# Optimization experiments

Measured on AMD Instinct MI355X. Metric: run time of the kernel, lower is better.

Reference implementation:

```python
import jax, jax.numpy as jnp
import numpy as np

T = 32          # timesteps
GAIN = 1.0      # input_gain
TAU = 2.0       # LIF membrane time constant
VTH = 1.0       # v_threshold
VRESET = 0.0    # v_reset (hard reset)
ALPHA = 2.0     # ATan surrogate alpha


@jax.custom_vjp
def heaviside_atan(x):
    # forward: Heaviside spike; backward: ATan surrogate gradient
    return (x >= 0).astype(x.dtype)

def _hs_fwd(x):
    return heaviside_atan(x), x

def _hs_bwd(x, g):
    # d/dx ATan surrogate: (alpha/2) / (1 + (pi/2 * alpha * x)^2)
    return (g * (ALPHA / 2.0) / (1.0 + (jnp.pi / 2.0 * ALPHA * x) ** 2),)

heaviside_atan.defvjp(_hs_fwd, _hs_bwd)


def lif_multistep(cur_seq):
    """Multi-step LIF over cur_seq [T, B, H]; hard reset, detach_reset=True."""
    def step(v, x):
        # charge: v = v + (x - (v - v_reset)) / tau
        v = v + (x - (v - VRESET)) / TAU
        spike = heaviside_atan(v - VTH)
        sd = jax.lax.stop_gradient(spike)  # detach_reset
        v = (1.0 - sd) * v + sd * VRESET   # hard reset
        return v, spike

    v0 = jnp.full(cur_seq.shape[1:], VRESET, dtype=cur_seq.dtype)
    _, spikes = jax.lax.scan(step, v0, cur_seq)
    return spikes


def setup_inputs() -> dict:
    key = jax.random.key(0)
    ks = jax.random.split(key, 4)

    def xavier(k, o, i):
        lim = np.sqrt(6.0 / (i + o)).astype(np.float32)
        return jax.random.uniform(k, (o, i), minval=-lim, maxval=lim, dtype=jnp.float32)

    x_flat = jax.random.uniform(ks[0], (512, 784), dtype=jnp.float32)
    W0 = xavier(ks[1], 1024, 784)
    b0 = jnp.zeros((1024,), jnp.float32)
    W1 = xavier(ks[2], 1024, 1024)
    b1 = jnp.zeros((1024,), jnp.float32)
    W2 = xavier(ks[3], 10, 1024)
    b2 = jnp.zeros((10,), jnp.float32)
    return {"x_flat": x_flat, "W0": W0, "b0": b0, "W1": W1, "b1": b1, "W2": W2, "b2": b2}


def reference(x_flat, W0, b0, W1, b1, W2, b2):
    # repeat_static_input: [B, 784] -> [T, B, 784]
    h = jnp.broadcast_to(x_flat * GAIN, (T,) + x_flat.shape)
    count = None
    for W, b in ((W0, b0), (W1, b1), (W2, b2)):
        cur = jnp.einsum('tbi,oi->tbo', h, W) + b  # fc over all timesteps
        spk = lif_multistep(cur)                   # [T, B, out]
        count = spk.sum(axis=0)                    # spike counts [B, out]
        h = spk
    # predict() returns argmax(count); return the final count (logits) here
    return count
```

## Files before the change

### kernel.cpp

```cpp
#include <hip/hip_runtime.h>
#include <hip/hip_bf16.h>
#include <stdint.h>


typedef __bf16 bf16x8 __attribute__((ext_vector_type(8)));
typedef float  f32x4  __attribute__((ext_vector_type(4)));

__device__ __forceinline__ void gload16(const void* g, void* l) {
  __builtin_amdgcn_global_load_lds((const __attribute__((address_space(1))) void*)g,
                                   (__attribute__((address_space(3))) void*)l,
                                   16, 0, 0);
}

__device__ __forceinline__ void bsplit3(float v, __hip_bfloat16& h,
                                        __hip_bfloat16& m, __hip_bfloat16& l) {
  h = __float2bfloat16(v);
  float r1 = v - __bfloat162float(h);
  m = __float2bfloat16(r1);
  float r2 = r1 - __bfloat162float(m);
  l = __float2bfloat16(r2);
}

__global__ __launch_bounds__(256) void prep_k(const float* __restrict__ x,
                                              const float* __restrict__ W0,
                                              const float* __restrict__ W1,
                                              __hip_bfloat16* __restrict__ Ax,
                                              __hip_bfloat16* __restrict__ Bw,
                                              float* __restrict__ W1T) {
  const int bid = blockIdx.x, tid = threadIdx.x;
  if (bid < 1600) {
    int i = bid * 256 + tid;
    int m = i / 800, k = i - m * 800;
    float v = (k < 784) ? x[(size_t)m * 784 + k] : 0.f;
    __hip_bfloat16 h, mm, l;
    bsplit3(v, h, mm, l);
    size_t base = (size_t)m * 4800;
    Ax[base + k] = h;         Ax[base + 800 + k] = h;
    Ax[base + 1600 + k] = mm; Ax[base + 2400 + k] = mm;
    Ax[base + 3200 + k] = h;  Ax[base + 4000 + k] = l;
  } else if (bid < 4800) {
    int i = (bid - 1600) * 256 + tid;
    int n = i / 800, k = i - n * 800;
    float v = (k < 784) ? W0[(size_t)n * 784 + k] : 0.f;
    __hip_bfloat16 h, mm, l;
    bsplit3(v, h, mm, l);
    size_t base = (size_t)n * 4800;
    Bw[base + k] = h;         Bw[base + 800 + k] = mm;
    Bw[base + 1600 + k] = h;  Bw[base + 2400 + k] = mm;
    Bw[base + 3200 + k] = l;  Bw[base + 4000 + k] = h;
  } else {
    __shared__ float t[32][33];
    int tt = bid - 4800;
    int c0 = (tt & 31) * 32, r0 = (tt >> 5) * 32;
    int lx = tid & 31, ly = tid >> 5;
#pragma unroll
    for (int i = 0; i < 32; i += 8)
      t[ly + i][lx] = W1[(size_t)(r0 + ly + i) * 1024 + (c0 + lx)];
    __syncthreads();
#pragma unroll
    for (int i = 0; i < 32; i += 8)
      W1T[(size_t)(c0 + ly + i) * 1024 + (r0 + lx)] = t[lx][ly + i];
  }
}

__global__ __launch_bounds__(256, 2) void gemm0_k(const __hip_bfloat16* __restrict__ A,
                                                  const __hip_bfloat16* __restrict__ B,
                                                  float* __restrict__ Cpart) {
  __shared__ __align__(16) __hip_bfloat16 As[128 * 32];
  __shared__ __align__(16) __hip_bfloat16 Bs[128 * 32];
  const int tid = threadIdx.x;
  const int wave = tid >> 6, lane = tid & 63, quad = lane >> 4, l16 = lane & 15;
  const int wm = (wave >> 1) * 64, wn = (wave & 1) * 64;
  const int mbase = blockIdx.x * 128, nbase = blockIdx.y * 128;
  const int kbase = blockIdx.z * 480;
  const int srow = lane >> 2;
  const int gq = (lane & 3) ^ ((lane >> 3) & 3);
  const int swz = (l16 >> 1) & 3;
  f32x4 acc[4][4] = {};
  for (int kk = kbase; kk < kbase + 480; kk += 32) {
#pragma unroll
    for (int r = 0; r < 2; ++r) {
      int grp = wave * 2 + r;
      gload16(A + (size_t)(mbase + grp * 16 + srow) * 4800 + kk + gq * 8,
              (char*)As + grp * 1024);
      gload16(B + (size_t)(nbase + grp * 16 + srow) * 4800 + kk + gq * 8,
              (char*)Bs + grp * 1024);
    }
    __syncthreads();
    const __bf16* Ab = (const __bf16*)As;
    const __bf16* Bb = (const __bf16*)Bs;
    bf16x8 af[4], bfr[4];
#pragma unroll
    for (int i = 0; i < 4; ++i)
      af[i] = *(const bf16x8*)(Ab + (wm + i * 16 + l16) * 32 + ((quad ^ swz) * 8));
#pragma unroll
    for (int j = 0; j < 4; ++j)
      bfr[j] = *(const bf16x8*)(Bb + (wn + j * 16 + l16) * 32 + ((quad ^ swz) * 8));
#pragma unroll
    for (int i = 0; i < 4; ++i)
#pragma unroll
      for (int j = 0; j < 4; ++j)
        acc[i][j] = __builtin_amdgcn_mfma_f32_16x16x32_bf16(af[i], bfr[j], acc[i][j], 0, 0, 0);
    __syncthreads();
  }
  float* Cz = Cpart + (size_t)blockIdx.z * 512 * 1024;
#pragma unroll
  for (int i = 0; i < 4; ++i)
#pragma unroll
    for (int j = 0; j < 4; ++j)
#pragma unroll
      for (int r = 0; r < 4; ++r) {
        int m = mbase + wm + i * 16 + quad * 4 + r;
        int n = nbase + wn + j * 16 + l16;
        Cz[(size_t)m * 1024 + n] = acc[i][j][r];
      }
}

__global__ __launch_bounds__(1024) void compact0_k(const float* __restrict__ Cpart,
                                                   const float* __restrict__ b0,
                                                   unsigned short* __restrict__ lidx16,
                                                   int* __restrict__ segs) {
  __shared__ int whist[16][33];
  __shared__ int clstot[33];
  __shared__ int clsofs[34];
  __shared__ int wofs[16][33];
  int b = blockIdx.x, o = threadIdx.x;
  int wave = o >> 6, lane = o & 63;
  float cur = 0.f;
#pragma unroll
  for (int z = 0; z < 10; ++z)
    cur += Cpart[(size_t)z * 512 * 1024 + (size_t)b * 1024 + o];
  cur += b0[o];
  float v = 0.f;
  unsigned word = 0u;
#pragma unroll
  for (int t = 0; t < 32; ++t) {
    v = v + (cur - v) * 0.5f;
    if (v >= 1.0f) { word |= 1u << t; v = 0.f; }
  }
  int n = word ? (__builtin_ctz(word) + 1) : 0;
  unsigned long long mymask = 0ull;
#pragma unroll 1
  for (int c = 1; c <= 32; ++c) {
    unsigned long long m = __ballot(n == c);
    if (lane == 0) whist[wave][c] = __popcll(m);
    if (n == c) mymask = m;
  }
  __syncthreads();
  if (o < 32) {
    int c = o + 1, s = 0;
#pragma unroll
    for (int w = 0; w < 16; ++w) s += whist[w][c];
    clstot[c] = s;
  }
  __syncthreads();
  if (o == 0) {
    int run = 0;
#pragma unroll
    for (int c = 1; c <= 32; ++c) { clsofs[c] = run; run += clstot[c]; }
    clsofs[33] = run;
  }
  __syncthreads();
  if (o < 32) {
    int c = o + 1, s = clsofs[c];
#pragma unroll
    for (int w = 0; w < 16; ++w) { wofs[w][c] = s; s += whist[w][c]; }
  }
  __syncthreads();
  if (n) {
    int pos = wofs[wave][n] + __popcll(mymask & ((1ull << lane) - 1ull));
    lidx16[(size_t)b * 1024 + pos] = (unsigned short)o;
  }
  if (o < 33) segs[b * 33 + o] = clsofs[o + 1];
}

__global__ __launch_bounds__(256) void layer1_k(const unsigned short* __restrict__ lidx16,
                                                const int* __restrict__ segs,
                                                const float* __restrict__ W1T,
                                                const float* __restrict__ b1,
                                                unsigned* __restrict__ l2idx,
                                                unsigned* __restrict__ l2wrd,
                                                int* __restrict__ n2t) {
  __shared__ unsigned short sidx[1024];
  __shared__ int sseg[33];
  __shared__ int wtot[4], wbase[4];
  const int tile = blockIdx.x, b = blockIdx.y;
  const int tid = threadIdx.x;
  const int o = tile * 256 + tid;
  if (tid < 33) sseg[tid] = segs[b * 33 + tid];
  __syncthreads();
  const int total = __builtin_amdgcn_readfirstlane(sseg[32]);
  for (int i = tid; i < total; i += 256)
    sidx[i] = lidx16[(size_t)b * 1024 + i];
  __syncthreads();
  float S[32];
#pragma unroll
  for (int c = 0; c < 32; ++c) {
    int j0 = __builtin_amdgcn_readfirstlane((c == 0) ? 0 : sseg[c - 1]);
    int j1 = __builtin_amdgcn_readfirstlane(sseg[c]);
    float s = 0.f;
    for (int j = j0; j < j1; ++j)
      s += W1T[(size_t)sidx[j] * 1024 + o];
    S[c] = s;
  }
  const float bias = b1[o];
  float v = 0.f;
  unsigned word = 0u;
#pragma unroll
  for (int t = 0; t < 32; ++t) {
    float cur = 0.f;
#pragma unroll
    for (int c = 1; c <= 32; ++c)
      if ((t + 1) % c == 0) cur += S[c - 1];
    float xc = cur + bias;
    v = v + (xc - v) * 0.5f;
    if (v >= 1.0f) { word |= 1u << t; v = 0.f; }
  }
  bool act = (word != 0u);
  unsigned long long m = __ballot(act);
  int wave = tid >> 6, lane = tid & 63;
  if (lane == 0) wtot[wave] = __popcll(m);
  __syncthreads();
  if (tid == 0) {
    int s = 0;
#pragma unroll
    for (int i = 0; i < 4; ++i) { wbase[i] = s; s += wtot[i]; }
    n2t[b * 4 + tile] = s;
  }
  __syncthreads();
  if (act) {
    int pos = wbase[wave] + __popcll(m & ((1ull << lane) - 1ull));
    l2idx[(size_t)b * 1024 + tile * 256 + pos] = (unsigned)o;
    l2wrd[(size_t)b * 1024 + tile * 256 + pos] = word;
  }
}

__global__ __launch_bounds__(320) void layer2_k(const unsigned* __restrict__ l2idx,
                                                const unsigned* __restrict__ l2wrd,
                                                const int* __restrict__ n2t,
                                                const float* __restrict__ W2,
                                                const float* __restrict__ b2,
                                                float* __restrict__ out) {
  __shared__ float sW2[10 * 1025];
  __shared__ unsigned sidx[1024], swrd[1024];
  __shared__ float scur[320];
  int b = blockIdx.x, tid = threadIdx.x;
  int cnt[4], ofs[4], mtot = 0;
#pragma unroll
  for (int s = 0; s < 4; ++s) {
    cnt[s] = n2t[b * 4 + s];
    ofs[s] = mtot;
    mtot += cnt[s];
  }
  for (int i = tid; i < 10240; i += 320)
    sW2[(i >> 10) * 1025 + (i & 1023)] = W2[i];
#pragma unroll
  for (int s = 0; s < 4; ++s)
    for (int i = tid; i < cnt[s]; i += 320) {
      sidx[ofs[s] + i] = l2idx[(size_t)b * 1024 + s * 256 + i];
      swrd[ofs[s] + i] = l2wrd[(size_t)b * 1024 + s * 256 + i];
    }
  __syncthreads();
  int t = tid / 10, c = tid - t * 10;
  float acc = 0.f;
  for (int j = 0; j < mtot; ++j) {
    unsigned wd = swrd[j];
    float wv = sW2[c * 1025 + sidx[j]];
    acc += ((wd >> t) & 1u) ? wv : 0.f;
  }
  scur[t * 10 + c] = acc;
  __syncthreads();
  if (tid < 10) {
    float v = 0.f, cnt2 = 0.f, bias = b2[tid];
#pragma unroll
    for (int tt = 0; tt < 32; ++tt) {
      float xc = scur[tt * 10 + tid] + bias;
      v = v + (xc - v) * 0.5f;
      if (v >= 1.0f) { cnt2 += 1.f; v = 0.f; }
    }
    out[(size_t)b * 10 + tid] = cnt2;
  }
}

extern "C" void kernel_launch(void* const* d_in, const int* in_sizes, int n_in,
                              void* d_out, int out_size, void* d_ws, size_t ws_size,
                              hipStream_t stream) {
  const float* x  = (const float*)d_in[0];
  const float* W0 = (const float*)d_in[1];
  const float* b0 = (const float*)d_in[2];
  const float* W1 = (const float*)d_in[3];
  const float* b1 = (const float*)d_in[4];
  const float* W2 = (const float*)d_in[5];
  const float* b2 = (const float*)d_in[6];
  float* out = (float*)d_out;

  char* ws = (char*)d_ws;
  size_t off = 0;
  auto alloc = [&](size_t bytes) -> char* {
    char* p = ws + off;
    off += (bytes + 255) & ~(size_t)255;
    return p;
  };
  __hip_bfloat16* Ax     = (__hip_bfloat16*)alloc((size_t)512 * 4800 * 2);
  __hip_bfloat16* Bw     = (__hip_bfloat16*)alloc((size_t)1024 * 4800 * 2);
  float*          Cpart  = (float*)alloc((size_t)10 * 512 * 1024 * 4);
  float*          W1T    = (float*)alloc((size_t)1024 * 1024 * 4);
  unsigned short* lidx16 = (unsigned short*)alloc((size_t)512 * 1024 * 2);
  int*            segs   = (int*)alloc((size_t)512 * 33 * 4);
  unsigned*       l2idx  = (unsigned*)alloc((size_t)512 * 1024 * 4);
  unsigned*       l2wrd  = (unsigned*)alloc((size_t)512 * 1024 * 4);
  int*            n2t    = (int*)alloc((size_t)512 * 4 * 4);
  (void)ws_size;

  prep_k<<<5824, 256, 0, stream>>>(x, W0, W1, Ax, Bw, W1T);
  gemm0_k<<<dim3(4, 8, 10), 256, 0, stream>>>(Ax, Bw, Cpart);
  compact0_k<<<512, 1024, 0, stream>>>(Cpart, b0, lidx16, segs);
  layer1_k<<<dim3(4, 512), 256, 0, stream>>>(lidx16, segs, W1T, b1, l2idx, l2wrd, n2t);
  layer2_k<<<512, 320, 0, stream>>>(l2idx, l2wrd, n2t, W2, b2, out);
}
```

Measured before the change: 117.7 us.

## Fuse bf16 split into GEMM loads and merge tail kernels into one

The GEMM now reads fp32 x and W0 directly, performs the three-way bf16 split on the fly, and writes swizzled tiles to LDS, replacing the separate prep pass and its large bf16 workspace. The W1 transpose runs as extra blocks of the same launch. Compaction, layer 1 and layer 2 are fused into one 1024-thread-per-batch kernel that keeps its intermediates in shared memory. This cuts kernel launches and global round-trips, but the GEMM loses asynchronous global-to-LDS loads and repeats the split arithmetic per tile, and layer 1 now runs on 512 blocks instead of 2048.

```diff
diff --git a/kernel.cpp b/kernel.cpp
--- a/kernel.cpp
+++ b/kernel.cpp
@@ -5,52 +5,30 @@
 
 typedef __bf16 bf16x8 __attribute__((ext_vector_type(8)));
 typedef float  f32x4  __attribute__((ext_vector_type(4)));
-
-__device__ __forceinline__ void gload16(const void* g, void* l) {
-  __builtin_amdgcn_global_load_lds((const __attribute__((address_space(1))) void*)g,
-                                   (__attribute__((address_space(3))) void*)l,
-                                   16, 0, 0);
+typedef unsigned short u16x8 __attribute__((ext_vector_type(8)));
+
+__device__ __forceinline__ unsigned short csel(float v, int sel) {
+  __hip_bfloat16 h = __float2bfloat16(v);
+  if (sel == 0) return __builtin_bit_cast(unsigned short, h);
+  float r1 = v - __bfloat162float(h);
+  __hip_bfloat16 m = __float2bfloat16(r1);
+  if (sel == 1) return __builtin_bit_cast(unsigned short, m);
+  float r2 = r1 - __bfloat162float(m);
+  __hip_bfloat16 l = __float2bfloat16(r2);
+  return __builtin_bit_cast(unsigned short, l);
 }
 
-__device__ __forceinline__ void bsplit3(float v, __hip_bfloat16& h,
-                                        __hip_bfloat16& m, __hip_bfloat16& l) {
-  h = __float2bfloat16(v);
-  float r1 = v - __bfloat162float(h);
-  m = __float2bfloat16(r1);
-  float r2 = r1 - __bfloat162float(m);
-  l = __float2bfloat16(r2);
-}
-
-__global__ __launch_bounds__(256) void prep_k(const float* __restrict__ x,
-                                              const float* __restrict__ W0,
-                                              const float* __restrict__ W1,
-                                              __hip_bfloat16* __restrict__ Ax,
-                                              __hip_bfloat16* __restrict__ Bw,
-                                              float* __restrict__ W1T) {
+__global__ __launch_bounds__(256, 2) void gemm0t_k(const float* __restrict__ x,
+                                                   const float* __restrict__ W0,
+                                                   const float* __restrict__ W1,
+                                                   float* __restrict__ W1T,
+                                                   float* __restrict__ Cpart) {
+  __shared__ __align__(16) char smem[16512];
   const int bid = blockIdx.x, tid = threadIdx.x;
-  if (bid < 1600) {
-    int i = bid * 256 + tid;
-    int m = i / 800, k = i - m * 800;
-    float v = (k < 784) ? x[(size_t)m * 784 + k] : 0.f;
-    __hip_bfloat16 h, mm, l;
-    bsplit3(v, h, mm, l);
-    size_t base = (size_t)m * 4800;
-    Ax[base + k] = h;         Ax[base + 800 + k] = h;
-    Ax[base + 1600 + k] = mm; Ax[base + 2400 + k] = mm;
-    Ax[base + 3200 + k] = h;  Ax[base + 4000 + k] = l;
-  } else if (bid < 4800) {
-    int i = (bid - 1600) * 256 + tid;
-    int n = i / 800, k = i - n * 800;
-    float v = (k < 784) ? W0[(size_t)n * 784 + k] : 0.f;
-    __hip_bfloat16 h, mm, l;
-    bsplit3(v, h, mm, l);
-    size_t base = (size_t)n * 4800;
-    Bw[base + k] = h;         Bw[base + 800 + k] = mm;
-    Bw[base + 1600 + k] = h;  Bw[base + 2400 + k] = mm;
-    Bw[base + 3200 + k] = l;  Bw[base + 4000 + k] = h;
-  } else {
-    __shared__ float t[32][33];
-    int tt = bid - 4800;
+
+  if (bid >= 320) {
+    float (*t)[33] = (float(*)[33])smem;
+    int tt = bid - 320;
     int c0 = (tt & 31) * 32, r0 = (tt >> 5) * 32;
     int lx = tid & 31, ly = tid >> 5;
 #pragma unroll
@@ -60,35 +38,74 @@
 #pragma unroll
     for (int i = 0; i < 32; i += 8)
       W1T[(size_t)(c0 + ly + i) * 1024 + (r0 + lx)] = t[lx][ly + i];
-  }
-}
-
-__global__ __launch_bounds__(256, 2) void gemm0_k(const __hip_bfloat16* __restrict__ A,
-                                                  const __hip_bfloat16* __restrict__ B,
-                                                  float* __restrict__ Cpart) {
-  __shared__ __align__(16) __hip_bfloat16 As[128 * 32];
-  __shared__ __align__(16) __hip_bfloat16 Bs[128 * 32];
-  const int tid = threadIdx.x;
+    return;
+  }
+
+  const int bx = bid & 3, by = (bid >> 2) & 7, bz = bid >> 5;
   const int wave = tid >> 6, lane = tid & 63, quad = lane >> 4, l16 = lane & 15;
   const int wm = (wave >> 1) * 64, wn = (wave & 1) * 64;
-  const int mbase = blockIdx.x * 128, nbase = blockIdx.y * 128;
-  const int kbase = blockIdx.z * 480;
-  const int srow = lane >> 2;
-  const int gq = (lane & 3) ^ ((lane >> 3) & 3);
+  const int mbase = bx * 128, nbase = by * 128, kbase = bz * 480;
   const int swz = (l16 >> 1) & 3;
+
+  const int r = tid >> 1, h = tid & 1;
+  const int sw = (r >> 1) & 3;
+  const int swap = sw & 1;
+  char* adst = smem + r * 64 + 32 * (h ^ (sw >> 1));
+  char* bdst = smem + 8192 + r * 64 + 32 * (h ^ (sw >> 1));
+  const float* xr = x + (size_t)(mbase + r) * 784;
+  const float* wr = W0 + (size_t)(nbase + r) * 784;
+
   f32x4 acc[4][4] = {};
+
   for (int kk = kbase; kk < kbase + 480; kk += 32) {
-#pragma unroll
-    for (int r = 0; r < 2; ++r) {
-      int grp = wave * 2 + r;
-      gload16(A + (size_t)(mbase + grp * 16 + srow) * 4800 + kk + gq * 8,
-              (char*)As + grp * 1024);
-      gload16(B + (size_t)(nbase + grp * 16 + srow) * 4800 + kk + gq * 8,
-              (char*)Bs + grp * 1024);
-    }
-    __syncthreads();
-    const __bf16* Ab = (const __bf16*)As;
-    const __bf16* Bb = (const __bf16*)Bs;
+    const int s = kk / 800;
+    const int k0 = kk - s * 800 + h * 16;
+    const int selA = (s == 2 || s == 3) ? 1 : ((s == 5) ? 2 : 0);
+    const int selB = (s == 1 || s == 3) ? 1 : ((s == 4) ? 2 : 0);
+    {
+      float v[16];
+#pragma unroll
+      for (int q = 0; q < 4; ++q) {
+        int kq = k0 + q * 4;
+        if (kq < 784) {
+          f32x4 t4 = *(const f32x4*)(xr + kq);
+          v[q*4+0] = t4[0]; v[q*4+1] = t4[1]; v[q*4+2] = t4[2]; v[q*4+3] = t4[3];
+        } else {
+          v[q*4+0] = 0.f; v[q*4+1] = 0.f; v[q*4+2] = 0.f; v[q*4+3] = 0.f;
+        }
+      }
+      u16x8 c0v, c1v;
+#pragma unroll
+      for (int j = 0; j < 8; ++j) c0v[j] = csel(v[j], selA);
+#pragma unroll
+      for (int j = 0; j < 8; ++j) c1v[j] = csel(v[8 + j], selA);
+      *(u16x8*)(adst + (swap ? 16 : 0)) = c0v;
+      *(u16x8*)(adst + (swap ? 0 : 16)) = c1v;
+    }
+    {
+      float v[16];
+#pragma unroll
+      for (int q = 0; q < 4; ++q) {
+        int kq = k0 + q * 4;
+        if (kq < 784) {
+          f32x4 t4 = *(const f32x4*)(wr + kq);
+          v[q*4+0] = t4[0]; v[q*4+1] = t4[1]; v[q*4+2] = t4[2]; v[q*4+3] = t4[3];
+        } else {
+          v[q*4+0] = 0.f; v[q*4+1] = 0.f; v[q*4+2] = 0.f; v[q*4+3] = 0.f;
+        }
+      }
+      u16x8 c0v, c1v;
+#pragma unroll
+      for (int j = 0; j < 8; ++j) c0v[j] = csel(v[j], selB);
+#pragma unroll
+      for (int j = 0; j < 8; ++j) c1v[j] = csel(v[8 + j], selB);
+      *(u16x8*)(bdst + (swap ? 16 : 0)) = c0v;
+      *(u16x8*)(bdst + (swap ? 0 : 16)) = c1v;
+    }
+    __syncthreads();
+
+    const __bf16* Ab = (const __bf16*)smem;
+    const __bf16* Bb = Ab + 128 * 32;
     bf16x8 af[4], bfr[4];
 #pragma unroll
     for (int i = 0; i < 4; ++i)
@@ -103,182 +120,163 @@
         acc[i][j] = __builtin_amdgcn_mfma_f32_16x16x32_bf16(af[i], bfr[j], acc[i][j], 0, 0, 0);
     __syncthreads();
   }
-  float* Cz = Cpart + (size_t)blockIdx.z * 512 * 1024;
+
+  float* Cz = Cpart + (size_t)bz * 512 * 1024;
 #pragma unroll
   for (int i = 0; i < 4; ++i)
 #pragma unroll
     for (int j = 0; j < 4; ++j)
 #pragma unroll
-      for (int r = 0; r < 4; ++r) {
-        int m = mbase + wm + i * 16 + quad * 4 + r;
+      for (int rr = 0; rr < 4; ++rr) {
+        int m = mbase + wm + i * 16 + quad * 4 + rr;
         int n = nbase + wn + j * 16 + l16;
-        Cz[(size_t)m * 1024 + n] = acc[i][j][r];
+        Cz[(size_t)m * 1024 + n] = acc[i][j][rr];
       }
 }
 
-__global__ __launch_bounds__(1024) void compact0_k(const float* __restrict__ Cpart,
-                                                   const float* __restrict__ b0,
-                                                   unsigned short* __restrict__ lidx16,
-                                                   int* __restrict__ segs) {
-  __shared__ int whist[16][33];
-  __shared__ int clstot[33];
-  __shared__ int clsofs[34];
-  __shared__ int wofs[16][33];
-  int b = blockIdx.x, o = threadIdx.x;
-  int wave = o >> 6, lane = o & 63;
-  float cur = 0.f;
-#pragma unroll
-  for (int z = 0; z < 10; ++z)
-    cur += Cpart[(size_t)z * 512 * 1024 + (size_t)b * 1024 + o];
-  cur += b0[o];
-  float v = 0.f;
-  unsigned word = 0u;
-#pragma unroll
-  for (int t = 0; t < 32; ++t) {
-    v = v + (cur - v) * 0.5f;
-    if (v >= 1.0f) { word |= 1u << t; v = 0.f; }
-  }
-  int n = word ? (__builtin_ctz(word) + 1) : 0;
-  unsigned long long mymask = 0ull;
+struct TailSM {
+  unsigned short sidx[1024];
+  int sseg[33];
+  int mtot;
+  unsigned l2i[1024];
+  unsigned l2w[1024];
+  union {
+    struct { int whist[16][33]; int clstot[33]; int clsofs[34]; int wofs[16][33]; } s3;
+    struct { int wtot[16]; int wbase[16]; } s4;
+    struct { float sW2[10 * 1025]; float scur[320]; } s5;
+  } u;
+};
+
+__global__ __launch_bounds__(1024) void tail_k(const float* __restrict__ Cpart,
+                                               const float* __restrict__ b0,
+                                               const float* __restrict__ W1T,
+                                               const float* __restrict__ b1,
+                                               const float* __restrict__ W2,
+                                               const float* __restrict__ b2,
+                                               float* __restrict__ out) {
+  __shared__ TailSM sm;
+  const int b = blockIdx.x, o = threadIdx.x;
+  const int wave = o >> 6, lane = o & 63;
+
+  {
+    float cur = 0.f;
+#pragma unroll
+    for (int z = 0; z < 10; ++z)
+      cur += Cpart[(size_t)z * 512 * 1024 + (size_t)b * 1024 + o];
+    cur += b0[o];
+    float v = 0.f;
+    unsigned word = 0u;
+#pragma unroll
+    for (int t = 0; t < 32; ++t) {
+      v = v + (cur - v) * 0.5f;
+      if (v >= 1.0f) { word |= 1u << t; v = 0.f; }
+    }
+    int n = word ? (__builtin_ctz(word) + 1) : 0;
+    unsigned long long mymask = 0ull;
 #pragma unroll 1
-  for (int c = 1; c <= 32; ++c) {
-    unsigned long long m = __ballot(n == c);
-    if (lane == 0) whist[wave][c] = __popcll(m);
-    if (n == c) mymask = m;
+    for (int c = 1; c <= 32; ++c) {
+      unsigned long long m = __ballot(n == c);
+      if (lane == 0) sm.u.s3.whist[wave][c] = __popcll(m);
+      if (n == c) mymask = m;
+    }
+    __syncthreads();
+    if (o < 32) {
+      int c = o + 1, s = 0;
+#pragma unroll
+      for (int w = 0; w < 16; ++w) s += sm.u.s3.whist[w][c];
+      sm.u.s3.clstot[c] = s;
+    }
+    __syncthreads();
+    if (o == 0) {
+      int run = 0;
+#pragma unroll
+      for (int c = 1; c <= 32; ++c) { sm.u.s3.clsofs[c] = run; run += sm.u.s3.clstot[c]; }
+      sm.u.s3.clsofs[33] = run;
+    }
+    __syncthreads();
+    if (o < 32) {
+      int c = o + 1, s = sm.u.s3.clsofs[c];
+#pragma unroll
+      for (int w = 0; w < 16; ++w) { sm.u.s3.wofs[w][c] = s; s += sm.u.s3.whist[w][c]; }
+    }
+    __syncthreads();
+    if (n) {
+      int pos = sm.u.s3.wofs[wave][n] + __popcll(mymask & ((1ull << lane) - 1ull));
+      sm.sidx[pos] = (unsigned short)o;
+    }
+    if (o < 33) sm.sseg[o] = sm.u.s3.clsofs[o + 1];
   }
   __syncthreads();
-  if (o < 32) {
-    int c = o + 1, s = 0;
-#pragma unroll
-    for (int w = 0; w < 16; ++w) s += whist[w][c];
-    clstot[c] = s;
+
+  {
+    float S[32];
+#pragma unroll
+    for (int c = 0; c < 32; ++c) {
+      int j0 = __builtin_amdgcn_readfirstlane((c == 0) ? 0 : sm.sseg[c - 1]);
+      int j1 = __builtin_amdgcn_readfirstlane(sm.sseg[c]);
+      float s = 0.f;
+      for (int j = j0; j < j1; ++j)
+        s += W1T[(size_t)sm.sidx[j] * 1024 + o];
+      S[c] = s;
+    }
+    const float bias = b1[o];
+    float v = 0.f;
+    unsigned word = 0u;
+#pragma unroll
+    for (int t = 0; t < 32; ++t) {
+      float cur = 0.f;
+#pragma unroll
+      for (int c = 1; c <= 32; ++c)
+        if ((t + 1) % c == 0) cur += S[c - 1];
+      float xc = cur + bias;
+      v = v + (xc - v) * 0.5f;
+      if (v >= 1.0f) { word |= 1u << t; v = 0.f; }
+    }
+    bool act = (word != 0u);
+    unsigned long long m = __ballot(act);
+    if (lane == 0) sm.u.s4.wtot[wave] = __popcll(m);
+    __syncthreads();
+    if (o == 0) {
+      int s = 0;
+#pragma unroll
+      for (int i = 0; i < 16; ++i) { sm.u.s4.wbase[i] = s; s += sm.u.s4.wtot[i]; }
+      sm.mtot = s;
+    }
+    __syncthreads();
+    if (act) {
+      int pos = sm.u.s4.wbase[wave] + __popcll(m & ((1ull << lane) - 1ull));
+      sm.l2i[pos] = (unsigned)o;
+      sm.l2w[pos] = word;
+    }
   }
   __syncthreads();
-  if (o == 0) {
-    int run = 0;
-#pragma unroll
-    for (int c = 1; c <= 32; ++c) { clsofs[c] = run; run += clstot[c]; }
-    clsofs[33] = run;
-  }
-  __syncthreads();
-  if (o < 32) {
-    int c = o + 1, s = clsofs[c];
-#pragma unroll
-    for (int w = 0; w < 16; ++w) { wofs[w][c] = s; s += whist[w][c]; }
-  }
-  __syncthreads();
-  if (n) {
-    int pos = wofs[wave][n] + __popcll(mymask & ((1ull << lane) - 1ull));
-    lidx16[(size_t)b * 1024 + pos] = (unsigned short)o;
-  }
-  if (o < 33) segs[b * 33 + o] = clsofs[o + 1];
-}
-
-__global__ __launch_bounds__(256) void layer1_k(const unsigned short* __restrict__ lidx16,
-                                                const int* __restrict__ segs,
-                                                const float* __restrict__ W1T,
-                                                const float* __restrict__ b1,
-                                                unsigned* __restrict__ l2idx,
-                                                unsigned* __restrict__ l2wrd,
-                                                int* __restrict__ n2t) {
-  __shared__ unsigned short sidx[1024];
-  __shared__ int sseg[33];
-  __shared__ int wtot[4], wbase[4];
-  const int tile = blockIdx.x, b = blockIdx.y;
-  const int tid = threadIdx.x;
-  const int o = tile * 256 + tid;
-  if (tid < 33) sseg[tid] = segs[b * 33 + tid];
-  __syncthreads();
-  const int total = __builtin_amdgcn_readfirstlane(sseg[32]);
-  for (int i = tid; i < total; i += 256)
-    sidx[i] = lidx16[(size_t)b * 1024 + i];
-  __syncthreads();
-  float S[32];
-#pragma unroll
-  for (int c = 0; c < 32; ++c) {
-    int j0 = __builtin_amdgcn_readfirstlane((c == 0) ? 0 : sseg[c - 1]);
-    int j1 = __builtin_amdgcn_readfirstlane(sseg[c]);
-    float s = 0.f;
-    for (int j = j0; j < j1; ++j)
-      s += W1T[(size_t)sidx[j] * 1024 + o];
-    S[c] = s;
-  }
-  const float bias = b1[o];
-  float v = 0.f;
-  unsigned word = 0u;
-#pragma unroll
-  for (int t = 0; t < 32; ++t) {
-    float cur = 0.f;
-#pragma unroll
-    for (int c = 1; c <= 32; ++c)
-      if ((t + 1) % c == 0) cur += S[c - 1];
-    float xc = cur + bias;
-    v = v + (xc - v) * 0.5f;
-    if (v >= 1.0f) { word |= 1u << t; v = 0.f; }
-  }
-  bool act = (word != 0u);
-  unsigned long long m = __ballot(act);
-  int wave = tid >> 6, lane = tid & 63;
-  if (lane == 0) wtot[wave] = __popcll(m);
-  __syncthreads();
-  if (tid == 0) {
-    int s = 0;
-#pragma unroll
-    for (int i = 0; i < 4; ++i) { wbase[i] = s; s += wtot[i]; }
-    n2t[b * 4 + tile] = s;
-  }
-  __syncthreads();
-  if (act) {
-    int pos = wbase[wave] + __popcll(m & ((1ull << lane) - 1ull));
-    l2idx[(size_t)b * 1024 + tile * 256 + pos] = (unsigned)o;
-    l2wrd[(size_t)b * 1024 + tile * 256 + pos] = word;
-  }
-}
-
-__global__ __launch_bounds__(320) void layer2_k(const unsigned* __restrict__ l2idx,
-                                                const unsigned* __restrict__ l2wrd,
-                                                const int* __restrict__ n2t,
-                                                const float* __restrict__ W2,
-                                                const float* __restrict__ b2,
-                                                float* __restrict__ out) {
-  __shared__ float sW2[10 * 1025];
-  __shared__ unsigned sidx[1024], swrd[1024];
-  __shared__ float scur[320];
-  int b = blockIdx.x, tid = threadIdx.x;
-  int cnt[4], ofs[4], mtot = 0;
-#pragma unroll
-  for (int s = 0; s < 4; ++s) {
-    cnt[s] = n2t[b * 4 + s];
-    ofs[s] = mtot;
-    mtot += cnt[s];
-  }
-  for (int i = tid; i < 10240; i += 320)
-    sW2[(i >> 10) * 1025 + (i & 1023)] = W2[i];
-#pragma unroll
-  for (int s = 0; s < 4; ++s)
-    for (int i = tid; i < cnt[s]; i += 320) {
-      sidx[ofs[s] + i] = l2idx[(size_t)b * 1024 + s * 256 + i];
-      swrd[ofs[s] + i] = l2wrd[(size_t)b * 1024 + s * 256 + i];
-    }
-  __syncthreads();
-  int t = tid / 10, c = tid - t * 10;
-  float acc = 0.f;
-  for (int j = 0; j < mtot; ++j) {
-    unsigned wd = swrd[j];
-    float wv = sW2[c * 1025 + sidx[j]];
-    acc += ((wd >> t) & 1u) ? wv : 0.f;
-  }
-  scur[t * 10 + c] = acc;
-  __syncthreads();
-  if (tid < 10) {
-    float v = 0.f, cnt2 = 0.f, bias = b2[tid];
-#pragma unroll
-    for (int tt = 0; tt < 32; ++tt) {
-      float xc = scur[tt * 10 + tid] + bias;
-      v = v + (xc - v) * 0.5f;
-      if (v >= 1.0f) { cnt2 += 1.f; v = 0.f; }
-    }
-    out[(size_t)b * 10 + tid] = cnt2;
+
+  {
+    for (int i = o; i < 10240; i += 1024)
+      sm.u.s5.sW2[(i >> 10) * 1025 + (i & 1023)] = W2[i];
+    __syncthreads();
+    const int mtot = sm.mtot;
+    if (o < 320) {
+      int t = o / 10, c = o - t * 10;
+      float acc = 0.f;
+      for (int j = 0; j < mtot; ++j) {
+        unsigned wd = sm.l2w[j];
+        float wv = sm.u.s5.sW2[c * 1025 + sm.l2i[j]];
+        acc += ((wd >> t) & 1u) ? wv : 0.f;
+      }
+      sm.u.s5.scur[o] = acc;
+    }
+    __syncthreads();
+    if (o < 10) {
+      float v = 0.f, cnt2 = 0.f, bias = b2[o];
+#pragma unroll
+      for (int tt = 0; tt < 32; ++tt) {
+        float xc = sm.u.s5.scur[tt * 10 + o] + bias;
+        v = v + (xc - v) * 0.5f;
+        if (v >= 1.0f) { cnt2 += 1.f; v = 0.f; }
+      }
+      out[(size_t)b * 10 + o] = cnt2;
+    }
   }
 }
 
@@ -301,20 +299,10 @@
     off += (bytes + 255) & ~(size_t)255;
     return p;
   };
-  __hip_bfloat16* Ax     = (__hip_bfloat16*)alloc((size_t)512 * 4800 * 2);
-  __hip_bfloat16* Bw     = (__hip_bfloat16*)alloc((size_t)1024 * 4800 * 2);
-  float*          Cpart  = (float*)alloc((size_t)10 * 512 * 1024 * 4);
-  float*          W1T    = (float*)alloc((size_t)1024 * 1024 * 4);
-  unsigned short* lidx16 = (unsigned short*)alloc((size_t)512 * 1024 * 2);
-  int*            segs   = (int*)alloc((size_t)512 * 33 * 4);
-  unsigned*       l2idx  = (unsigned*)alloc((size_t)512 * 1024 * 4);
-  unsigned*       l2wrd  = (unsigned*)alloc((size_t)512 * 1024 * 4);
-  int*            n2t    = (int*)alloc((size_t)512 * 4 * 4);
+  float* Cpart = (float*)alloc((size_t)10 * 512 * 1024 * 4);
+  float* W1T   = (float*)alloc((size_t)1024 * 1024 * 4);
   (void)ws_size;
 
-  prep_k<<<5824, 256, 0, stream>>>(x, W0, W1, Ax, Bw, W1T);
-  gemm0_k<<<dim3(4, 8, 10), 256, 0, stream>>>(Ax, Bw, Cpart);
-  compact0_k<<<512, 1024, 0, stream>>>(Cpart, b0, lidx16, segs);
-  layer1_k<<<dim3(4, 512), 256, 0, stream>>>(lidx16, segs, W1T, b1, l2idx, l2wrd, n2t);
-  layer2_k<<<512, 320, 0, stream>>>(l2idx, l2wrd, n2t, W2, b2, out);
+  gemm0t_k<<<1344, 256, 0, stream>>>(x, W0, W1, W1T, Cpart);
+  tail_k<<<512, 1024, 0, stream>>>(Cpart, b0, W1T, b1, W2, b2, out);
 }
```

After: 125.0 us. 1.06x slower.

## Fuse bf16 three-way split into GEMM0 loads and merge W1 transpose launch

Applied to the files above, without the earlier changes.

Drops the separate prep kernel that expanded x and W0 into 6-segment bf16 split buffers. The GEMM now reads fp32 rows directly, computes the needed hi/mid/lo bf16 component on the fly, and writes it into swizzled LDS. The W1 transpose runs as extra blocks in the same launch. This removes one launch and the write and reread of the large split buffers, but the conversion work is redone per tile and the asynchronous global-to-LDS loads become synchronous register staging.

```diff
diff --git a/kernel.cpp b/kernel.cpp
--- a/kernel.cpp
+++ b/kernel.cpp
@@ -5,52 +5,30 @@
 
 typedef __bf16 bf16x8 __attribute__((ext_vector_type(8)));
 typedef float  f32x4  __attribute__((ext_vector_type(4)));
-
-__device__ __forceinline__ void gload16(const void* g, void* l) {
-  __builtin_amdgcn_global_load_lds((const __attribute__((address_space(1))) void*)g,
-                                   (__attribute__((address_space(3))) void*)l,
-                                   16, 0, 0);
-}
-
-__device__ __forceinline__ void bsplit3(float v, __hip_bfloat16& h,
-                                        __hip_bfloat16& m, __hip_bfloat16& l) {
-  h = __float2bfloat16(v);
+typedef unsigned short u16x8 __attribute__((ext_vector_type(8)));
+
+__device__ __forceinline__ unsigned short csel(float v, int sel) {
+  __hip_bfloat16 h = __float2bfloat16(v);
+  if (sel == 0) return __builtin_bit_cast(unsigned short, h);
   float r1 = v - __bfloat162float(h);
-  m = __float2bfloat16(r1);
+  __hip_bfloat16 m = __float2bfloat16(r1);
+  if (sel == 1) return __builtin_bit_cast(unsigned short, m);
   float r2 = r1 - __bfloat162float(m);
-  l = __float2bfloat16(r2);
-}
-
-__global__ __launch_bounds__(256) void prep_k(const float* __restrict__ x,
-                                              const float* __restrict__ W0,
-                                              const float* __restrict__ W1,
-                                              __hip_bfloat16* __restrict__ Ax,
-                                              __hip_bfloat16* __restrict__ Bw,
-                                              float* __restrict__ W1T) {
+  __hip_bfloat16 l = __float2bfloat16(r2);
+  return __builtin_bit_cast(unsigned short, l);
+}
+
+__global__ __launch_bounds__(256, 2) void gemm0t_k(const float* __restrict__ x,
+                                                   const float* __restrict__ W0,
+                                                   const float* __restrict__ W1,
+                                                   float* __restrict__ W1T,
+                                                   float* __restrict__ Cpart) {
+  __shared__ __align__(16) char smem[16512];
   const int bid = blockIdx.x, tid = threadIdx.x;
-  if (bid < 1600) {
-    int i = bid * 256 + tid;
-    int m = i / 800, k = i - m * 800;
-    float v = (k < 784) ? x[(size_t)m * 784 + k] : 0.f;
-    __hip_bfloat16 h, mm, l;
-    bsplit3(v, h, mm, l);
-    size_t base = (size_t)m * 4800;
-    Ax[base + k] = h;         Ax[base + 800 + k] = h;
-    Ax[base + 1600 + k] = mm; Ax[base + 2400 + k] = mm;
-    Ax[base + 3200 + k] = h;  Ax[base + 4000 + k] = l;
-  } else if (bid < 4800) {
-    int i = (bid - 1600) * 256 + tid;
-    int n = i / 800, k = i - n * 800;
-    float v = (k < 784) ? W0[(size_t)n * 784 + k] : 0.f;
-    __hip_bfloat16 h, mm, l;
-    bsplit3(v, h, mm, l);
-    size_t base = (size_t)n * 4800;
-    Bw[base + k] = h;         Bw[base + 800 + k] = mm;
-    Bw[base + 1600 + k] = h;  Bw[base + 2400 + k] = mm;
-    Bw[base + 3200 + k] = l;  Bw[base + 4000 + k] = h;
-  } else {
-    __shared__ float t[32][33];
-    int tt = bid - 4800;
+
+  if (bid >= 320) {
+    float (*t)[33] = (float(*)[33])smem;
+    int tt = bid - 320;
     int c0 = (tt & 31) * 32, r0 = (tt >> 5) * 32;
     int lx = tid & 31, ly = tid >> 5;
 #pragma unroll
@@ -60,35 +38,74 @@
 #pragma unroll
     for (int i = 0; i < 32; i += 8)
       W1T[(size_t)(c0 + ly + i) * 1024 + (r0 + lx)] = t[lx][ly + i];
-  }
-}
-
-__global__ __launch_bounds__(256, 2) void gemm0_k(const __hip_bfloat16* __restrict__ A,
-                                                  const __hip_bfloat16* __restrict__ B,
-                                                  float* __restrict__ Cpart) {
-  __shared__ __align__(16) __hip_bfloat16 As[128 * 32];
-  __shared__ __align__(16) __hip_bfloat16 Bs[128 * 32];
-  const int tid = threadIdx.x;
+    return;
+  }
+
+  const int bx = bid & 3, by = (bid >> 2) & 7, bz = bid >> 5;
   const int wave = tid >> 6, lane = tid & 63, quad = lane >> 4, l16 = lane & 15;
   const int wm = (wave >> 1) * 64, wn = (wave & 1) * 64;
-  const int mbase = blockIdx.x * 128, nbase = blockIdx.y * 128;
-  const int kbase = blockIdx.z * 480;
-  const int srow = lane >> 2;
-  const int gq = (lane & 3) ^ ((lane >> 3) & 3);
+  const int mbase = bx * 128, nbase = by * 128, kbase = bz * 480;
   const int swz = (l16 >> 1) & 3;
+
+  const int r = tid >> 1, h = tid & 1;
+  const int sw = (r >> 1) & 3;
+  const int swap = sw & 1;
+  char* adst = smem + r * 64 + 32 * (h ^ (sw >> 1));
+  char* bdst = smem + 8192 + r * 64 + 32 * (h ^ (sw >> 1));
+  const float* xr = x + (size_t)(mbase + r) * 784;
+  const float* wr = W0 + (size_t)(nbase + r) * 784;
+
   f32x4 acc[4][4] = {};
+
   for (int kk = kbase; kk < kbase + 480; kk += 32) {
-#pragma unroll
-    for (int r = 0; r < 2; ++r) {
-      int grp = wave * 2 + r;
-      gload16(A + (size_t)(mbase + grp * 16 + srow) * 4800 + kk + gq * 8,
-              (char*)As + grp * 1024);
-      gload16(B + (size_t)(nbase + grp * 16 + srow) * 4800 + kk + gq * 8,
-              (char*)Bs + grp * 1024);
+    const int s = kk / 800;
+    const int k0 = kk - s * 800 + h * 16;
+    const int selA = (s == 2 || s == 3) ? 1 : ((s == 5) ? 2 : 0);
+    const int selB = (s == 1 || s == 3) ? 1 : ((s == 4) ? 2 : 0);
+    {
+      float v[16];
+#pragma unroll
+      for (int q = 0; q < 4; ++q) {
+        int kq = k0 + q * 4;
+        if (kq < 784) {
+          f32x4 t4 = *(const f32x4*)(xr + kq);
+          v[q*4+0] = t4[0]; v[q*4+1] = t4[1]; v[q*4+2] = t4[2]; v[q*4+3] = t4[3];
+        } else {
+          v[q*4+0] = 0.f; v[q*4+1] = 0.f; v[q*4+2] = 0.f; v[q*4+3] = 0.f;
+        }
+      }
+      u16x8 c0v, c1v;
+#pragma unroll
+      for (int j = 0; j < 8; ++j) c0v[j] = csel(v[j], selA);
+#pragma unroll
+      for (int j = 0; j < 8; ++j) c1v[j] = csel(v[8 + j], selA);
+      *(u16x8*)(adst + (swap ? 16 : 0)) = c0v;
+      *(u16x8*)(adst + (swap ? 0 : 16)) = c1v;
+    }
+    {
+      float v[16];
+#pragma unroll
+      for (int q = 0; q < 4; ++q) {
+        int kq = k0 + q * 4;
+        if (kq < 784) {
+          f32x4 t4 = *(const f32x4*)(wr + kq);
+          v[q*4+0] = t4[0]; v[q*4+1] = t4[1]; v[q*4+2] = t4[2]; v[q*4+3] = t4[3];
+        } else {
+          v[q*4+0] = 0.f; v[q*4+1] = 0.f; v[q*4+2] = 0.f; v[q*4+3] = 0.f;
+        }
+      }
+      u16x8 c0v, c1v;
+#pragma unroll
+      for (int j = 0; j < 8; ++j) c0v[j] = csel(v[j], selB);
+#pragma unroll
+      for (int j = 0; j < 8; ++j) c1v[j] = csel(v[8 + j], selB);
+      *(u16x8*)(bdst + (swap ? 16 : 0)) = c0v;
+      *(u16x8*)(bdst + (swap ? 0 : 16)) = c1v;
     }
     __syncthreads();
-    const __bf16* Ab = (const __bf16*)As;
-    const __bf16* Bb = (const __bf16*)Bs;
+
+    const __bf16* Ab = (const __bf16*)smem;
+    const __bf16* Bb = Ab + 128 * 32;
     bf16x8 af[4], bfr[4];
 #pragma unroll
     for (int i = 0; i < 4; ++i)
@@ -103,16 +120,17 @@
         acc[i][j] = __builtin_amdgcn_mfma_f32_16x16x32_bf16(af[i], bfr[j], acc[i][j], 0, 0, 0);
     __syncthreads();
   }
-  float* Cz = Cpart + (size_t)blockIdx.z * 512 * 1024;
+
+  float* Cz = Cpart + (size_t)bz * 512 * 1024;
 #pragma unroll
   for (int i = 0; i < 4; ++i)
 #pragma unroll
     for (int j = 0; j < 4; ++j)
 #pragma unroll
-      for (int r = 0; r < 4; ++r) {
-        int m = mbase + wm + i * 16 + quad * 4 + r;
+      for (int rr = 0; rr < 4; ++rr) {
+        int m = mbase + wm + i * 16 + quad * 4 + rr;
         int n = nbase + wn + j * 16 + l16;
-        Cz[(size_t)m * 1024 + n] = acc[i][j][r];
+        Cz[(size_t)m * 1024 + n] = acc[i][j][rr];
       }
 }
 
@@ -301,8 +319,6 @@
     off += (bytes + 255) & ~(size_t)255;
     return p;
   };
-  __hip_bfloat16* Ax     = (__hip_bfloat16*)alloc((size_t)512 * 4800 * 2);
-  __hip_bfloat16* Bw     = (__hip_bfloat16*)alloc((size_t)1024 * 4800 * 2);
   float*          Cpart  = (float*)alloc((size_t)10 * 512 * 1024 * 4);
   float*          W1T    = (float*)alloc((size_t)1024 * 1024 * 4);
   unsigned short* lidx16 = (unsigned short*)alloc((size_t)512 * 1024 * 2);
@@ -312,8 +328,7 @@
   int*            n2t    = (int*)alloc((size_t)512 * 4 * 4);
   (void)ws_size;
 
-  prep_k<<<5824, 256, 0, stream>>>(x, W0, W1, Ax, Bw, W1T);
-  gemm0_k<<<dim3(4, 8, 10), 256, 0, stream>>>(Ax, Bw, Cpart);
+  gemm0t_k<<<1344, 256, 0, stream>>>(x, W0, W1, W1T, Cpart);
   compact0_k<<<512, 1024, 0, stream>>>(Cpart, b0, lidx16, segs);
   layer1_k<<<dim3(4, 512), 256, 0, stream>>>(lidx16, segs, W1T, b1, l2idx, l2wrd, n2t);
   layer2_k<<<512, 320, 0, stream>>>(l2idx, l2wrd, n2t, W2, b2, out);
```

Measured after the change: 130.9 us. 1.11x slower.
